# Performance work log

Hardware: AMD Instinct MI355X
Metric: run time of the kernel (lower is better)

Reference implementation:

```python
import jax, jax.numpy as jnp
import numpy as np

B = 65536   # batch (agent-timesteps)
NN = 16     # neighbors per agent
NO = 32     # obstacles per agent
SD = 4      # state_dim_per_agent
D_ROBOT = 0.3
D_OBST = 0.5
B_GAMMA = 0.01
B_EXPH = 1.0
A_MIN, A_MAX = -2.0, 2.0
PHI_MIN, PHI_MAX = -2.0, 2.0


def _mlp2(h, W1, b1, W2, b2):
    # DeepSet sub-network: activation between layers, linear last (matches
    # 'for layer in layers[:-1]: x = act(layer(x)); x = layers[-1](x)')
    return jax.nn.relu(h @ W1 + b1) @ W2 + b2


def setup_inputs() -> dict:
    key = jax.random.key(0)
    ks = jax.random.split(key, 24)
    own = jax.random.normal(ks[0], (B, SD), dtype=jnp.float32)
    # relative positions with |component| in [0.5, 2.0] so norms exceed D_* (barrier well-defined)
    npos = jax.random.uniform(ks[1], (B, NN, 2), minval=0.5, maxval=2.0) * jnp.sign(jax.random.normal(ks[2], (B, NN, 2)))
    nvel = 0.1 * jax.random.normal(ks[3], (B, NN, 2))
    neigh = jnp.concatenate([npos, nvel], axis=-1).reshape(B, 4 * NN)
    opos = (jax.random.uniform(ks[4], (B, NO, 2), minval=0.5, maxval=2.0) * jnp.sign(jax.random.normal(ks[5], (B, NO, 2)))).reshape(B, 2 * NO)
    x = jnp.concatenate([jnp.full((B, 1), float(NN), dtype=jnp.float32), own, neigh, opos], axis=1)
    noise = 0.05 * jax.random.normal(ks[6], (B, 2), dtype=jnp.float32)  # the 0.05*N(0,1) action noise, made deterministic

    def lin(k, i, o):
        return 0.1 * jax.random.normal(k, (i, o), dtype=jnp.float32)

    return {
        'x': x, 'noise': noise,
        # neighbor DeepSet: phi 4->64->16, rho 16->64->8
        'pnW1': lin(ks[7], 4, 64),  'pnb1': jnp.zeros((64,), jnp.float32),
        'pnW2': lin(ks[8], 64, 16), 'pnb2': jnp.zeros((16,), jnp.float32),
        'rnW1': lin(ks[9], 16, 64), 'rnb1': jnp.zeros((64,), jnp.float32),
        'rnW2': lin(ks[10], 64, 8), 'rnb2': jnp.zeros((8,), jnp.float32),
        # obstacle DeepSet: phi 2->64->16, rho 16->64->8
        'poW1': lin(ks[11], 2, 64),  'pob1': jnp.zeros((64,), jnp.float32),
        'poW2': lin(ks[12], 64, 16), 'pob2': jnp.zeros((16,), jnp.float32),
        'roW1': lin(ks[13], 16, 64), 'rob1': jnp.zeros((64,), jnp.float32),
        'roW2': lin(ks[14], 64, 8),  'rob2': jnp.zeros((8,), jnp.float32),
        # psi: 18 -> 64 -> 64 -> 2
        'psW1': lin(ks[15], 18, 64), 'psb1': jnp.zeros((64,), jnp.float32),
        'psW2': lin(ks[16], 64, 64), 'psb2': jnp.zeros((64,), jnp.float32),
        'psW3': lin(ks[17], 64, 2),  'psb3': jnp.zeros((2,), jnp.float32),
    }


def reference(x, noise,
              pnW1, pnb1, pnW2, pnb2, rnW1, rnb1, rnW2, rnb2,
              poW1, pob1, poW2, pob2, roW1, rob1, roW2, rob2,
              psW1, psb1, psW2, psb2, psW3, psb3):
    b = x.shape[0]
    neigh = x[:, 5:5 + 4 * NN].reshape(b, NN, 4)   # per-neighbor relative state
    obst = x[:, 5 + 4 * NN:].reshape(b, NO, 2)      # per-obstacle relative pos

    # 'empty' (learned) action: DeepSets + psi MLP
    rho_n = _mlp2(_mlp2(neigh, pnW1, pnb1, pnW2, pnb2).sum(axis=1), rnW1, rnb1, rnW2, rnb2)
    rho_o = _mlp2(_mlp2(obst, poW1, pob1, poW2, pob2).sum(axis=1), roW1, rob1, roW2, rob2)
    g = x[:, 1:3]
    h = jnp.concatenate([rho_n, rho_o, g], axis=1)
    h = jax.nn.relu(h @ psW1 + psb1)
    h = jax.nn.relu(h @ psW2 + psb2)
    h = jnp.tanh(h @ psW3 + psb3)
    empty = (h + 1.0) / 2.0 * (PHI_MAX - PHI_MIN) + PHI_MIN

    # barrier terms, vectorized over all neighbors/obstacles at once:
    # A = b_gamma * P * ||P||^-1 * (||P|| - D)^(-b_exph), summed over edges
    def barrier_sum(P, D):
        nrm = jnp.linalg.norm(P, axis=-1, keepdims=True)   # [b, E, 1]
        H = nrm - D
        return (B_GAMMA * P / (nrm * H ** B_EXPH)).sum(axis=1)

    bar = barrier_sum(-neigh[..., :2], D_ROBOT) + barrier_sum(-obst, D_OBST)

    a = jnp.tanh(empty + bar + noise)
    return (a + 1.0) / 2.0 * (A_MAX - A_MIN) + A_MIN
```

## Files before the change

### kernel.cpp

```cpp
#include <hip/hip_runtime.h>

#define NN 16
#define NO 32
#define XCOLS 133

typedef _Float16 h8v __attribute__((ext_vector_type(8)));
typedef _Float16 h2 __attribute__((ext_vector_type(2)));
typedef float f4v __attribute__((ext_vector_type(4)));
typedef unsigned ui4 __attribute__((ext_vector_type(4)));
typedef float f2u __attribute__((ext_vector_type(2), aligned(4)));

static __device__ __forceinline__ f4v MFMA(h8v a, h8v b, f4v c) {
    return __builtin_amdgcn_mfma_f32_16x16x32_f16(a, b, c, 0, 0, 0);
}
static __device__ __forceinline__ unsigned pkbits(float a, float b) {
    return __builtin_bit_cast(unsigned, __builtin_amdgcn_cvt_pkrtz(a, b));
}
static __device__ __forceinline__ h2 u2h(unsigned v) { return __builtin_bit_cast(h2, v); }

__global__ void prep_frags(
    const float* __restrict__ pnW1, const float* __restrict__ pnW2,
    const float* __restrict__ rnW1, const float* __restrict__ rnW2,
    const float* __restrict__ poW1, const float* __restrict__ poW2,
    const float* __restrict__ roW1, const float* __restrict__ roW2,
    const float* __restrict__ psW1, const float* __restrict__ psW2,
    const float* __restrict__ psW3, unsigned* __restrict__ ws)
{
    const float* Ws[11] = {pnW1,pnW2,rnW1,rnW2,poW1,poW2,roW1,roW2,psW1,psW2,psW3};
    const int Kr[11]   = {4,64,16,64,2,64,16,64,18,64,64};
    const int Nr[11]   = {64,16,64,8,64,16,64,8,64,64,2};
    const int nkc[11]  = {1,2,1,2,1,2,1,2,1,2,2};
    const int nnt[11]  = {4,1,4,1,4,1,4,1,4,4,1};
    const int base[11] = {0,1024,1536,2560,3072,4096,4608,5632,6144,7168,9216};

    const int gid = blockIdx.x * 256 + threadIdx.x;
    int start = 0;
    #pragma unroll
    for (int a2 = 0; a2 < 11; ++a2) {
        const int n = nkc[a2] * nnt[a2] * 256;
        if (gid >= start && gid < start + n) {
            const int i = gid - start;
            const float* Wm = Ws[a2];
            const int K = Kr[a2], N = Nr[a2], nt_n = nnt[a2];
            const int d = i & 3, lane = (i >> 2) & 63, t = i >> 8;
            const int nt = t % nt_n, kc = t / nt_n;
            const int k = kc * 32 + 8 * (lane >> 4) + 2 * d;
            const int col = nt * 16 + (lane & 15);
            const float v0 = (k     < K && col < N) ? Wm[(k    ) * N + col] : 0.f;
            const float v1 = (k + 1 < K && col < N) ? Wm[(k + 1) * N + col] : 0.f;
            ws[base[a2] + i] = pkbits(v0, v1);
        }
        start += n;
    }
}

__global__ __launch_bounds__(64, 4) void barrier_net_kernel(
    const float* __restrict__ x, const float* __restrict__ noise,
    const float* __restrict__ pnb1, const float* __restrict__ pnb2,
    const float* __restrict__ rnb1, const float* __restrict__ rnb2,
    const float* __restrict__ pob1, const float* __restrict__ pob2,
    const float* __restrict__ rob1, const float* __restrict__ rob2,
    const float* __restrict__ psb1, const float* __restrict__ psb2,
    const float* __restrict__ psb3,
    const unsigned* __restrict__ wsu, float* __restrict__ out)
{
    __shared__ unsigned XS[16 * 66];
    __shared__ _Float16 W[3136];

    const int l = threadIdx.x;
    const int r = l & 15;
    const int g = l >> 4;
    const int eb = blockIdx.x * 16;

    float* barf = (float*)(W + 3072);
    const h8v* FB = (const h8v*)wsu;

    {
        const float* base = x + (size_t)eb * XCOLS;
        f2u raw[16];
        #pragma unroll
        for (int it = 0; it < 16; ++it)
            raw[it] = *(const f2u*)(base + (size_t)it * XCOLS + 5 + 2 * l);
        f2u graw = {0.f, 0.f};
        if (l < 16) graw = *(const f2u*)(base + (size_t)l * XCOLS + 1);
        #pragma unroll
        for (int it = 0; it < 16; ++it)
            XS[it * 66 + l] = pkbits(raw[it][0], raw[it][1]);
        if (l < 16) XS[l * 66 + 64] = pkbits(graw[0], graw[1]);
    }

    {
        unsigned* z = (unsigned*)(W + 2048);
        #pragma unroll
        for (int i = 0; i < 8; ++i) z[l + 64 * i] = 0u;
    }

    const int rowb = r * 66;
    const int sw8 = (r & 7) << 3;
    const int sw4 = (r & 3) << 3;

    {
        float bq0 = 0.f, bq1 = 0.f;
        #pragma unroll
        for (int jj = 0; jj < 4; ++jj) {
            const h2 v = u2h(XS[rowb + 2 * (4 * g + jj)]);
            const float v0 = (float)v[0], v1 = (float)v[1];
            const float nrm = sqrtf(v0*v0 + v1*v1);
            const float cc = 0.01f * __builtin_amdgcn_rcpf(nrm * (nrm - 0.3f));
            bq0 -= cc * v0; bq1 -= cc * v1;
        }
        #pragma unroll
        for (int jj = 0; jj < 8; ++jj) {
            const h2 v = u2h(XS[rowb + 32 + 8 * g + jj]);
            const float v0 = (float)v[0], v1 = (float)v[1];
            const float nrm = sqrtf(v0*v0 + v1*v1);
            const float cc = 0.01f * __builtin_amdgcn_rcpf(nrm * (nrm - 0.5f));
            bq0 -= cc * v0; bq1 -= cc * v1;
        }
        bq0 += __shfl_xor(bq0, 16); bq0 += __shfl_xor(bq0, 32);
        bq1 += __shfl_xor(bq1, 16); bq1 += __shfl_xor(bq1, 32);
        if (g == 0) { barf[2*r] = bq0; barf[2*r + 1] = bq1; }
    }

    {
        const h8v B0 = FB[0*64 + l], B1 = FB[1*64 + l];
        const h8v B2 = FB[2*64 + l], B3 = FB[3*64 + l];
        const f4v c0 = {pnb1[r], pnb1[r], pnb1[r], pnb1[r]};
        const f4v c1 = {pnb1[16+r], pnb1[16+r], pnb1[16+r], pnb1[16+r]};
        const f4v c2 = {pnb1[32+r], pnb1[32+r], pnb1[32+r], pnb1[32+r]};
        const f4v c3 = {pnb1[48+r], pnb1[48+r], pnb1[48+r], pnb1[48+r]};
        f4v s0 = {0,0,0,0}, s1 = {0,0,0,0}, s2 = {0,0,0,0}, s3 = {0,0,0,0};
        #pragma unroll 4
        for (int j = 0; j < NN; ++j) {
            const uint2 np = *(const uint2*)&XS[rowb + 2 * j];
            ui4 au = {np.x, np.y, 0u, 0u};
            const h8v a = __builtin_bit_cast(h8v, au);
            const f4v d0 = MFMA(a, B0, c0);
            const f4v d1 = MFMA(a, B1, c1);
            const f4v d2 = MFMA(a, B2, c2);
            const f4v d3 = MFMA(a, B3, c3);
            #pragma unroll
            for (int q = 0; q < 4; ++q) {
                s0[q] += fmaxf(d0[q], 0.f); s1[q] += fmaxf(d1[q], 0.f);
                s2[q] += fmaxf(d2[q], 0.f); s3[q] += fmaxf(d3[q], 0.f);
            }
        }
        #pragma unroll
        for (int q = 0; q < 4; ++q) {
            const int e = 4 * g + q;
            const int m = (e & 7) << 3;
            W[e*64 + (( 0 + r) ^ m)] = (_Float16)s0[q];
            W[e*64 + ((16 + r) ^ m)] = (_Float16)s1[q];
            W[e*64 + ((32 + r) ^ m)] = (_Float16)s2[q];
            W[e*64 + ((48 + r) ^ m)] = (_Float16)s3[q];
        }
    }

    {
        const h8v B0 = FB[768 + 0*64 + l], B1 = FB[768 + 1*64 + l];
        const h8v B2 = FB[768 + 2*64 + l], B3 = FB[768 + 3*64 + l];
        const f4v c0 = {pob1[r], pob1[r], pob1[r], pob1[r]};
        const f4v c1 = {pob1[16+r], pob1[16+r], pob1[16+r], pob1[16+r]};
        const f4v c2 = {pob1[32+r], pob1[32+r], pob1[32+r], pob1[32+r]};
        const f4v c3 = {pob1[48+r], pob1[48+r], pob1[48+r], pob1[48+r]};
        f4v s0 = {0,0,0,0}, s1 = {0,0,0,0}, s2 = {0,0,0,0}, s3 = {0,0,0,0};
        #pragma unroll 2
        for (int t = 0; t < 16; ++t) {
            const uint2 op = *(const uint2*)&XS[rowb + 32 + 2 * t];
            ui4 au0 = {op.x, 0u, 0u, 0u};
            ui4 au1 = {op.y, 0u, 0u, 0u};
            const h8v a0 = __builtin_bit_cast(h8v, au0);
            const h8v a1 = __builtin_bit_cast(h8v, au1);
            const f4v d0 = MFMA(a0, B0, c0); const f4v e0 = MFMA(a1, B0, c0);
            const f4v d1 = MFMA(a0, B1, c1); const f4v e1 = MFMA(a1, B1, c1);
            const f4v d2 = MFMA(a0, B2, c2); const f4v e2 = MFMA(a1, B2, c2);
            const f4v d3 = MFMA(a0, B3, c3); const f4v e3 = MFMA(a1, B3, c3);
            #pragma unroll
            for (int q = 0; q < 4; ++q) {
                s0[q] += fmaxf(d0[q], 0.f) + fmaxf(e0[q], 0.f);
                s1[q] += fmaxf(d1[q], 0.f) + fmaxf(e1[q], 0.f);
                s2[q] += fmaxf(d2[q], 0.f) + fmaxf(e2[q], 0.f);
                s3[q] += fmaxf(d3[q], 0.f) + fmaxf(e3[q], 0.f);
            }
        }
        #pragma unroll
        for (int q = 0; q < 4; ++q) {
            const int e = 4 * g + q;
            const int m = (e & 7) << 3;
            W[1024 + e*64 + (( 0 + r) ^ m)] = (_Float16)s0[q];
            W[1024 + e*64 + ((16 + r) ^ m)] = (_Float16)s1[q];
            W[1024 + e*64 + ((32 + r) ^ m)] = (_Float16)s2[q];
            W[1024 + e*64 + ((48 + r) ^ m)] = (_Float16)s3[q];
        }
    }

    {
        h8v a0 = *(const h8v*)&W[r*64 + (( 0 + 8*g) ^ sw8)];
        h8v a1 = *(const h8v*)&W[r*64 + ((32 + 8*g) ^ sw8)];
        h8v b0 = FB[256 + 0*64 + l];
        h8v b1 = FB[256 + 1*64 + l];
        const float bb = 16.f * pnb2[r];
        f4v c = {bb, bb, bb, bb};
        f4v d = MFMA(a1, b1, MFMA(a0, b0, c));
        #pragma unroll
        for (int q = 0; q < 4; ++q) {
            const int row = 4 * g + q;
            W[2048 + row*32 + (r ^ ((row&3)<<3))] = (_Float16)d[q];
        }
    }
    {
        h8v a = *(const h8v*)&W[2048 + r*32 + ((8*g) ^ sw4)];
        #pragma unroll
        for (int nt = 0; nt < 4; ++nt) {
            h8v b = FB[384 + nt*64 + l];
            const float bb = rnb1[16*nt + r];
            f4v c = {bb, bb, bb, bb};
            f4v d = MFMA(a, b, c);
            #pragma unroll
            for (int q = 0; q < 4; ++q) {
                const int row = 4 * g + q;
                W[row*64 + ((16*nt + r) ^ ((row&7)<<3))] = (_Float16)fmaxf(d[q], 0.f);
            }
        }
    }
    {
        h8v a0 = *(const h8v*)&W[r*64 + (( 0 + 8*g) ^ sw8)];
        h8v a1 = *(const h8v*)&W[r*64 + ((32 + 8*g) ^ sw8)];
        h8v b0 = FB[640 + 0*64 + l];
        h8v b1 = FB[640 + 1*64 + l];
        const float bb = (r < 8) ? rnb2[r & 7] : 0.f;
        f4v c = {bb, bb, bb, bb};
        f4v d = MFMA(a1, b1, MFMA(a0, b0, c));
        if (r < 8) {
            #pragma unroll
            for (int q = 0; q < 4; ++q) {
                const int row = 4 * g + q;
                W[2560 + row*32 + (r ^ ((row&3)<<3))] = (_Float16)d[q];
            }
        }
    }
    {
        h8v a0 = *(const h8v*)&W[1024 + r*64 + (( 0 + 8*g) ^ sw8)];
        h8v a1 = *(const h8v*)&W[1024 + r*64 + ((32 + 8*g) ^ sw8)];
        h8v b0 = FB[1024 + 0*64 + l];
        h8v b1 = FB[1024 + 1*64 + l];
        const float bb = 32.f * pob2[r];
        f4v c = {bb, bb, bb, bb};
        f4v d = MFMA(a1, b1, MFMA(a0, b0, c));
        #pragma unroll
        for (int q = 0; q < 4; ++q) {
            const int row = 4 * g + q;
            W[2048 + row*32 + (r ^ ((row&3)<<3))] = (_Float16)d[q];
        }
    }
    {
        h8v a = *(const h8v*)&W[2048 + r*32 + ((8*g) ^ sw4)];
        #pragma unroll
        for (int nt = 0; nt < 4; ++nt) {
            h8v b = FB[1152 + nt*64 + l];
            const float bb = rob1[16*nt + r];
            f4v c = {bb, bb, bb, bb};
            f4v d = MFMA(a, b, c);
            #pragma unroll
            for (int q = 0; q < 4; ++q) {
                const int row = 4 * g + q;
                W[row*64 + ((16*nt + r) ^ ((row&7)<<3))] = (_Float16)fmaxf(d[q], 0.f);
            }
        }
    }
    {
        h8v a0 = *(const h8v*)&W[r*64 + (( 0 + 8*g) ^ sw8)];
        h8v a1 = *(const h8v*)&W[r*64 + ((32 + 8*g) ^ sw8)];
        h8v b0 = FB[1408 + 0*64 + l];
        h8v b1 = FB[1408 + 1*64 + l];
        const float bb = (r < 8) ? rob2[r & 7] : 0.f;
        f4v c = {bb, bb, bb, bb};
        f4v d = MFMA(a1, b1, MFMA(a0, b0, c));
        if (r < 8) {
            #pragma unroll
            for (int q = 0; q < 4; ++q) {
                const int row = 4 * g + q;
                W[2560 + row*32 + ((8 + r) ^ ((row&3)<<3))] = (_Float16)d[q];
            }
        }
    }
    if (g == 0) {
        const h2 gv = u2h(XS[rowb + 64]);
        W[2560 + r*32 + (16 ^ sw4)] = gv[0];
        W[2560 + r*32 + (17 ^ sw4)] = gv[1];
    }
    {
        h8v a = *(const h8v*)&W[2560 + r*32 + ((8*g) ^ sw4)];
        #pragma unroll
        for (int nt = 0; nt < 4; ++nt) {
            h8v b = FB[1536 + nt*64 + l];
            const float bb = psb1[16*nt + r];
            f4v c = {bb, bb, bb, bb};
            f4v d = MFMA(a, b, c);
            #pragma unroll
            for (int q = 0; q < 4; ++q) {
                const int row = 4 * g + q;
                W[1024 + row*64 + ((16*nt + r) ^ ((row&7)<<3))] = (_Float16)fmaxf(d[q], 0.f);
            }
        }
    }
    {
        h8v a0 = *(const h8v*)&W[1024 + r*64 + (( 0 + 8*g) ^ sw8)];
        h8v a1 = *(const h8v*)&W[1024 + r*64 + ((32 + 8*g) ^ sw8)];
        #pragma unroll
        for (int nt = 0; nt < 4; ++nt) {
            h8v b0 = FB[1792 + (0*4 + nt)*64 + l];
            h8v b1 = FB[1792 + (1*4 + nt)*64 + l];
            const float bb = psb2[16*nt + r];
            f4v c = {bb, bb, bb, bb};
            f4v d = MFMA(a1, b1, MFMA(a0, b0, c));
            #pragma unroll
            for (int q = 0; q < 4; ++q) {
                const int row = 4 * g + q;
                W[row*64 + ((16*nt + r) ^ ((row&7)<<3))] = (_Float16)fmaxf(d[q], 0.f);
            }
        }
    }
    f4v dOut;
    {
        h8v a0 = *(const h8v*)&W[r*64 + (( 0 + 8*g) ^ sw8)];
        h8v a1 = *(const h8v*)&W[r*64 + ((32 + 8*g) ^ sw8)];
        h8v b0 = FB[2304 + 0*64 + l];
        h8v b1 = FB[2304 + 1*64 + l];
        const float bb = (r < 2) ? psb3[r & 1] : 0.f;
        f4v c = {bb, bb, bb, bb};
        dOut = MFMA(a1, b1, MFMA(a0, b0, c));
    }
    if (r < 2) {
        #pragma unroll
        for (int q = 0; q < 4; ++q) {
            const int e = 4 * g + q;
            const float o = dOut[q];
            const float bar = barf[e*2 + r];
            const float nz = noise[2 * (size_t)(eb + e) + r];
            const float av = tanhf(2.f * tanhf(o) + bar + nz);
            out[2 * (size_t)(eb + e) + r] = 2.f * av;
        }
    }
}

extern "C" void kernel_launch(void* const* d_in, const int* in_sizes, int n_in,
                              void* d_out, int out_size, void* d_ws, size_t ws_size,
                              hipStream_t stream) {
    const float* x    = (const float*)d_in[0];
    const float* nz   = (const float*)d_in[1];
    const float* pnW1 = (const float*)d_in[2];
    const float* pnb1 = (const float*)d_in[3];
    const float* pnW2 = (const float*)d_in[4];
    const float* pnb2 = (const float*)d_in[5];
    const float* rnW1 = (const float*)d_in[6];
    const float* rnb1 = (const float*)d_in[7];
    const float* rnW2 = (const float*)d_in[8];
    const float* rnb2 = (const float*)d_in[9];
    const float* poW1 = (const float*)d_in[10];
    const float* pob1 = (const float*)d_in[11];
    const float* poW2 = (const float*)d_in[12];
    const float* pob2 = (const float*)d_in[13];
    const float* roW1 = (const float*)d_in[14];
    const float* rob1 = (const float*)d_in[15];
    const float* roW2 = (const float*)d_in[16];
    const float* rob2 = (const float*)d_in[17];
    const float* psW1 = (const float*)d_in[18];
    const float* psb1 = (const float*)d_in[19];
    const float* psW2 = (const float*)d_in[20];
    const float* psb2 = (const float*)d_in[21];
    const float* psW3 = (const float*)d_in[22];
    const float* psb3 = (const float*)d_in[23];

    unsigned* ws = (unsigned*)d_ws;
    hipLaunchKernelGGL(prep_frags, dim3(38), dim3(256), 0, stream,
        pnW1, pnW2, rnW1, rnW2, poW1, poW2, roW1, roW2, psW1, psW2, psW3, ws);

    const int b = in_sizes[0] / XCOLS;
    hipLaunchKernelGGL(barrier_net_kernel, dim3(b / 16), dim3(64), 0, stream,
        x, nz, pnb1, pnb2, rnb1, rnb2, pob1, pob2, rob1, rob2,
        psb1, psb2, psb3, ws, (float*)d_out);
}
```

Baseline: 44.68 us.

## Split each 16-agent tile across two wavefronts with barrier-synchronized stages

Each block now runs two wavefronts on the same 16 agents. The phi-layer MFMA column tiles, the barrier sums and the psi layers are split between them, and the neighbor and obstacle rho branches run in parallel, one on each wave. The aim is to shorten the serial per-wave MFMA chain and add latency hiding. The cost is several __syncthreads, a larger shared buffer, and idle half-waves during the final single-wave stage.

```diff
diff --git a/kernel.cpp b/kernel.cpp
--- a/kernel.cpp
+++ b/kernel.cpp
@@ -54,7 +54,16 @@
     }
 }
 
-__global__ __launch_bounds__(64, 4) void barrier_net_kernel(
+#define SN  0
+#define SO  1024
+#define PNN 2048
+#define PNO 2560
+#define HBF 3072
+#define BARA 3584
+#define BARB 3648
+#define XSF 3712
+
+__global__ __launch_bounds__(128, 8) void barrier_net_kernel(
     const float* __restrict__ x, const float* __restrict__ noise,
     const float* __restrict__ pnb1, const float* __restrict__ pnb2,
     const float* __restrict__ rnb1, const float* __restrict__ rnb2,
@@ -64,54 +73,72 @@
     const float* __restrict__ psb3,
     const unsigned* __restrict__ wsu, float* __restrict__ out)
 {
-    __shared__ unsigned XS[16 * 66];
-    __shared__ _Float16 W[3136];
-
-    const int l = threadIdx.x;
+    __shared__ _Float16 S[5824];
+    unsigned* XS = (unsigned*)S + (XSF / 2);
+    float* barfA = (float*)(S + BARA);
+    float* barfB = (float*)(S + BARB);
+
+    const int tid = threadIdx.x;
+    const int l = tid & 63;
+    const int w = tid >> 6;
     const int r = l & 15;
     const int g = l >> 4;
     const int eb = blockIdx.x * 16;
 
-    float* barf = (float*)(W + 3072);
     const h8v* FB = (const h8v*)wsu;
-
-    {
-        const float* base = x + (size_t)eb * XCOLS;
-        f2u raw[16];
-        #pragma unroll
-        for (int it = 0; it < 16; ++it)
-            raw[it] = *(const f2u*)(base + (size_t)it * XCOLS + 5 + 2 * l);
-        f2u graw = {0.f, 0.f};
-        if (l < 16) graw = *(const f2u*)(base + (size_t)l * XCOLS + 1);
-        #pragma unroll
-        for (int it = 0; it < 16; ++it)
-            XS[it * 66 + l] = pkbits(raw[it][0], raw[it][1]);
-        if (l < 16) XS[l * 66 + 64] = pkbits(graw[0], graw[1]);
-    }
-
-    {
-        unsigned* z = (unsigned*)(W + 2048);
-        #pragma unroll
-        for (int i = 0; i < 8; ++i) z[l + 64 * i] = 0u;
-    }
-
-    const int rowb = r * 66;
     const int sw8 = (r & 7) << 3;
     const int sw4 = (r & 3) << 3;
+    const int nt0 = 2 * w, nt1 = 2 * w + 1;
+
+    {
+        unsigned* z = (unsigned*)(S + PNN);
+        #pragma unroll
+        for (int i = 0; i < 6; ++i) z[tid + 128 * i] = 0u;
+    }
+    {
+        const float* base = x + (size_t)eb * XCOLS;
+        f2u raw[8];
+        #pragma unroll
+        for (int i = 0; i < 8; ++i) {
+            const int idx = i * 128 + tid;
+            const int ee = idx >> 6, cp = idx & 63;
+            raw[i] = *(const f2u*)(base + (size_t)ee * XCOLS + 5 + 2 * cp);
+        }
+        #pragma unroll
+        for (int i = 0; i < 8; ++i) {
+            const int idx = i * 128 + tid;
+            const int ee = idx >> 6, cp = idx & 63;
+            XS[ee * 66 + cp] = pkbits(raw[i][0], raw[i][1]);
+        }
+        if (tid < 16) {
+            const f2u graw = *(const f2u*)(base + (size_t)tid * XCOLS + 1);
+            XS[tid * 66 + 64] = pkbits(graw[0], graw[1]);
+        }
+    }
+    __syncthreads();
+
+    const int rowb = r * 66;
+
+    if (tid < 16) {
+        const h2 gv = u2h(XS[tid * 66 + 64]);
+        const int m = (tid & 3) << 3;
+        S[HBF + tid * 32 + (16 ^ m)] = gv[0];
+        S[HBF + tid * 32 + (17 ^ m)] = gv[1];
+    }
 
     {
         float bq0 = 0.f, bq1 = 0.f;
         #pragma unroll
-        for (int jj = 0; jj < 4; ++jj) {
-            const h2 v = u2h(XS[rowb + 2 * (4 * g + jj)]);
+        for (int jj = 0; jj < 2; ++jj) {
+            const h2 v = u2h(XS[rowb + 2 * (8 * w + 2 * g + jj)]);
             const float v0 = (float)v[0], v1 = (float)v[1];
             const float nrm = sqrtf(v0*v0 + v1*v1);
             const float cc = 0.01f * __builtin_amdgcn_rcpf(nrm * (nrm - 0.3f));
             bq0 -= cc * v0; bq1 -= cc * v1;
         }
         #pragma unroll
-        for (int jj = 0; jj < 8; ++jj) {
-            const h2 v = u2h(XS[rowb + 32 + 8 * g + jj]);
+        for (int jj = 0; jj < 4; ++jj) {
+            const h2 v = u2h(XS[rowb + 32 + 16 * w + 4 * g + jj]);
             const float v0 = (float)v[0], v1 = (float)v[1];
             const float nrm = sqrtf(v0*v0 + v1*v1);
             const float cc = 0.01f * __builtin_amdgcn_rcpf(nrm * (nrm - 0.5f));
@@ -119,17 +146,18 @@
         }
         bq0 += __shfl_xor(bq0, 16); bq0 += __shfl_xor(bq0, 32);
         bq1 += __shfl_xor(bq1, 16); bq1 += __shfl_xor(bq1, 32);
-        if (g == 0) { barf[2*r] = bq0; barf[2*r + 1] = bq1; }
-    }
-
-    {
-        const h8v B0 = FB[0*64 + l], B1 = FB[1*64 + l];
-        const h8v B2 = FB[2*64 + l], B3 = FB[3*64 + l];
-        const f4v c0 = {pnb1[r], pnb1[r], pnb1[r], pnb1[r]};
-        const f4v c1 = {pnb1[16+r], pnb1[16+r], pnb1[16+r], pnb1[16+r]};
-        const f4v c2 = {pnb1[32+r], pnb1[32+r], pnb1[32+r], pnb1[32+r]};
-        const f4v c3 = {pnb1[48+r], pnb1[48+r], pnb1[48+r], pnb1[48+r]};
-        f4v s0 = {0,0,0,0}, s1 = {0,0,0,0}, s2 = {0,0,0,0}, s3 = {0,0,0,0};
+        if (g == 0) {
+            float* bf = w ? barfB : barfA;
+            bf[2*r] = bq0; bf[2*r + 1] = bq1;
+        }
+    }
+
+    {
+        const h8v B0 = FB[nt0 * 64 + l], B1 = FB[nt1 * 64 + l];
+        const float b0s = pnb1[16*nt0 + r], b1s = pnb1[16*nt1 + r];
+        const f4v c0 = {b0s, b0s, b0s, b0s};
+        const f4v c1 = {b1s, b1s, b1s, b1s};
+        f4v s0 = {0,0,0,0}, s1 = {0,0,0,0};
         #pragma unroll 4
         for (int j = 0; j < NN; ++j) {
             const uint2 np = *(const uint2*)&XS[rowb + 2 * j];
@@ -137,178 +165,172 @@
             const h8v a = __builtin_bit_cast(h8v, au);
             const f4v d0 = MFMA(a, B0, c0);
             const f4v d1 = MFMA(a, B1, c1);
-            const f4v d2 = MFMA(a, B2, c2);
-            const f4v d3 = MFMA(a, B3, c3);
-            #pragma unroll
-            for (int q = 0; q < 4; ++q) {
-                s0[q] += fmaxf(d0[q], 0.f); s1[q] += fmaxf(d1[q], 0.f);
-                s2[q] += fmaxf(d2[q], 0.f); s3[q] += fmaxf(d3[q], 0.f);
+            #pragma unroll
+            for (int q = 0; q < 4; ++q) {
+                s0[q] += fmaxf(d0[q], 0.f);
+                s1[q] += fmaxf(d1[q], 0.f);
             }
         }
         #pragma unroll
         for (int q = 0; q < 4; ++q) {
             const int e = 4 * g + q;
             const int m = (e & 7) << 3;
-            W[e*64 + (( 0 + r) ^ m)] = (_Float16)s0[q];
-            W[e*64 + ((16 + r) ^ m)] = (_Float16)s1[q];
-            W[e*64 + ((32 + r) ^ m)] = (_Float16)s2[q];
-            W[e*64 + ((48 + r) ^ m)] = (_Float16)s3[q];
-        }
-    }
-
-    {
-        const h8v B0 = FB[768 + 0*64 + l], B1 = FB[768 + 1*64 + l];
-        const h8v B2 = FB[768 + 2*64 + l], B3 = FB[768 + 3*64 + l];
-        const f4v c0 = {pob1[r], pob1[r], pob1[r], pob1[r]};
-        const f4v c1 = {pob1[16+r], pob1[16+r], pob1[16+r], pob1[16+r]};
-        const f4v c2 = {pob1[32+r], pob1[32+r], pob1[32+r], pob1[32+r]};
-        const f4v c3 = {pob1[48+r], pob1[48+r], pob1[48+r], pob1[48+r]};
-        f4v s0 = {0,0,0,0}, s1 = {0,0,0,0}, s2 = {0,0,0,0}, s3 = {0,0,0,0};
+            S[SN + e*64 + ((16*nt0 + r) ^ m)] = (_Float16)s0[q];
+            S[SN + e*64 + ((16*nt1 + r) ^ m)] = (_Float16)s1[q];
+        }
+    }
+
+    {
+        const h8v B0 = FB[768 + nt0 * 64 + l], B1 = FB[768 + nt1 * 64 + l];
+        const float b0s = pob1[16*nt0 + r], b1s = pob1[16*nt1 + r];
+        const f4v c0 = {b0s, b0s, b0s, b0s};
+        const f4v c1 = {b1s, b1s, b1s, b1s};
+        f4v s0 = {0,0,0,0}, s1 = {0,0,0,0};
         #pragma unroll 2
         for (int t = 0; t < 16; ++t) {
             const uint2 op = *(const uint2*)&XS[rowb + 32 + 2 * t];
-            ui4 au0 = {op.x, 0u, 0u, 0u};
-            ui4 au1 = {op.y, 0u, 0u, 0u};
-            const h8v a0 = __builtin_bit_cast(h8v, au0);
-            const h8v a1 = __builtin_bit_cast(h8v, au1);
+            ui4 a0u = {op.x, 0u, 0u, 0u};
+            ui4 a1u = {op.y, 0u, 0u, 0u};
+            const h8v a0 = __builtin_bit_cast(h8v, a0u);
+            const h8v a1 = __builtin_bit_cast(h8v, a1u);
             const f4v d0 = MFMA(a0, B0, c0); const f4v e0 = MFMA(a1, B0, c0);
             const f4v d1 = MFMA(a0, B1, c1); const f4v e1 = MFMA(a1, B1, c1);
-            const f4v d2 = MFMA(a0, B2, c2); const f4v e2 = MFMA(a1, B2, c2);
-            const f4v d3 = MFMA(a0, B3, c3); const f4v e3 = MFMA(a1, B3, c3);
             #pragma unroll
             for (int q = 0; q < 4; ++q) {
                 s0[q] += fmaxf(d0[q], 0.f) + fmaxf(e0[q], 0.f);
                 s1[q] += fmaxf(d1[q], 0.f) + fmaxf(e1[q], 0.f);
-                s2[q] += fmaxf(d2[q], 0.f) + fmaxf(e2[q], 0.f);
-                s3[q] += fmaxf(d3[q], 0.f) + fmaxf(e3[q], 0.f);
             }
         }
         #pragma unroll
         for (int q = 0; q < 4; ++q) {
             const int e = 4 * g + q;
             const int m = (e & 7) << 3;
-            W[1024 + e*64 + (( 0 + r) ^ m)] = (_Float16)s0[q];
-            W[1024 + e*64 + ((16 + r) ^ m)] = (_Float16)s1[q];
-            W[1024 + e*64 + ((32 + r) ^ m)] = (_Float16)s2[q];
-            W[1024 + e*64 + ((48 + r) ^ m)] = (_Float16)s3[q];
-        }
-    }
-
-    {
-        h8v a0 = *(const h8v*)&W[r*64 + (( 0 + 8*g) ^ sw8)];
-        h8v a1 = *(const h8v*)&W[r*64 + ((32 + 8*g) ^ sw8)];
-        h8v b0 = FB[256 + 0*64 + l];
-        h8v b1 = FB[256 + 1*64 + l];
-        const float bb = 16.f * pnb2[r];
-        f4v c = {bb, bb, bb, bb};
-        f4v d = MFMA(a1, b1, MFMA(a0, b0, c));
+            S[SO + e*64 + ((16*nt0 + r) ^ m)] = (_Float16)s0[q];
+            S[SO + e*64 + ((16*nt1 + r) ^ m)] = (_Float16)s1[q];
+        }
+    }
+    __syncthreads();
+
+    if (w == 0) {
+        {
+            h8v a0 = *(const h8v*)&S[SN + r*64 + (( 0 + 8*g) ^ sw8)];
+            h8v a1 = *(const h8v*)&S[SN + r*64 + ((32 + 8*g) ^ sw8)];
+            h8v b0 = FB[256 + 0*64 + l];
+            h8v b1 = FB[256 + 1*64 + l];
+            const float bb = 16.f * pnb2[r];
+            f4v c = {bb, bb, bb, bb};
+            f4v d = MFMA(a1, b1, MFMA(a0, b0, c));
+            #pragma unroll
+            for (int q = 0; q < 4; ++q) {
+                const int row = 4 * g + q;
+                S[PNN + row*32 + (r ^ ((row&3)<<3))] = (_Float16)d[q];
+            }
+        }
+        {
+            h8v a = *(const h8v*)&S[PNN + r*32 + ((8*g) ^ sw4)];
+            #pragma unroll
+            for (int nt = 0; nt < 4; ++nt) {
+                h8v b = FB[384 + nt*64 + l];
+                const float bb = rnb1[16*nt + r];
+                f4v c = {bb, bb, bb, bb};
+                f4v d = MFMA(a, b, c);
+                #pragma unroll
+                for (int q = 0; q < 4; ++q) {
+                    const int row = 4 * g + q;
+                    S[SN + row*64 + ((16*nt + r) ^ ((row&7)<<3))] = (_Float16)fmaxf(d[q], 0.f);
+                }
+            }
+        }
+        {
+            h8v a0 = *(const h8v*)&S[SN + r*64 + (( 0 + 8*g) ^ sw8)];
+            h8v a1 = *(const h8v*)&S[SN + r*64 + ((32 + 8*g) ^ sw8)];
+            h8v b0 = FB[640 + 0*64 + l];
+            h8v b1 = FB[640 + 1*64 + l];
+            const float bb = (r < 8) ? rnb2[r & 7] : 0.f;
+            f4v c = {bb, bb, bb, bb};
+            f4v d = MFMA(a1, b1, MFMA(a0, b0, c));
+            if (r < 8) {
+                #pragma unroll
+                for (int q = 0; q < 4; ++q) {
+                    const int row = 4 * g + q;
+                    S[HBF + row*32 + (r ^ ((row&3)<<3))] = (_Float16)d[q];
+                }
+            }
+        }
+    } else {
+        {
+            h8v a0 = *(const h8v*)&S[SO + r*64 + (( 0 + 8*g) ^ sw8)];
+            h8v a1 = *(const h8v*)&S[SO + r*64 + ((32 + 8*g) ^ sw8)];
+            h8v b0 = FB[1024 + 0*64 + l];
+            h8v b1 = FB[1024 + 1*64 + l];
+            const float bb = 32.f * pob2[r];
+            f4v c = {bb, bb, bb, bb};
+            f4v d = MFMA(a1, b1, MFMA(a0, b0, c));
+            #pragma unroll
+            for (int q = 0; q < 4; ++q) {
+                const int row = 4 * g + q;
+                S[PNO + row*32 + (r ^ ((row&3)<<3))] = (_Float16)d[q];
+            }
+        }
+        {
+            h8v a = *(const h8v*)&S[PNO + r*32 + ((8*g) ^ sw4)];
+            #pragma unroll
+            for (int nt = 0; nt < 4; ++nt) {
+                h8v b = FB[1152 + nt*64 + l];
+                const float bb = rob1[16*nt + r];
+                f4v c = {bb, bb, bb, bb};
+                f4v d = MFMA(a, b, c);
+                #pragma unroll
+                for (int q = 0; q < 4; ++q) {
+                    const int row = 4 * g + q;
+                    S[SO + row*64 + ((16*nt + r) ^ ((row&7)<<3))] = (_Float16)fmaxf(d[q], 0.f);
+                }
+            }
+        }
+        {
+            h8v a0 = *(const h8v*)&S[SO + r*64 + (( 0 + 8*g) ^ sw8)];
+            h8v a1 = *(const h8v*)&S[SO + r*64 + ((32 + 8*g) ^ sw8)];
+            h8v b0 = FB[1408 + 0*64 + l];
+            h8v b1 = FB[1408 + 1*64 + l];
+            const float bb = (r < 8) ? rob2[r & 7] : 0.f;
+            f4v c = {bb, bb, bb, bb};
+            f4v d = MFMA(a1, b1, MFMA(a0, b0, c));
+            if (r < 8) {
+                #pragma unroll
+                for (int q = 0; q < 4; ++q) {
+                    const int row = 4 * g + q;
+                    S[HBF + row*32 + ((8 + r) ^ ((row&3)<<3))] = (_Float16)d[q];
+                }
+            }
+        }
+    }
+    __syncthreads();
+
+    {
+        h8v a = *(const h8v*)&S[HBF + r*32 + ((8*g) ^ sw4)];
+        h8v b0 = FB[1536 + nt0*64 + l];
+        h8v b1 = FB[1536 + nt1*64 + l];
+        const float b0s = psb1[16*nt0 + r], b1s = psb1[16*nt1 + r];
+        f4v c0 = {b0s, b0s, b0s, b0s};
+        f4v c1 = {b1s, b1s, b1s, b1s};
+        f4v d0 = MFMA(a, b0, c0);
+        f4v d1 = MFMA(a, b1, c1);
         #pragma unroll
         for (int q = 0; q < 4; ++q) {
             const int row = 4 * g + q;
-            W[2048 + row*32 + (r ^ ((row&3)<<3))] = (_Float16)d[q];
-        }
-    }
-    {
-        h8v a = *(const h8v*)&W[2048 + r*32 + ((8*g) ^ sw4)];
-        #pragma unroll
-        for (int nt = 0; nt < 4; ++nt) {
-            h8v b = FB[384 + nt*64 + l];
-            const float bb = rnb1[16*nt + r];
-            f4v c = {bb, bb, bb, bb};
-            f4v d = MFMA(a, b, c);
-            #pragma unroll
-            for (int q = 0; q < 4; ++q) {
-                const int row = 4 * g + q;
-                W[row*64 + ((16*nt + r) ^ ((row&7)<<3))] = (_Float16)fmaxf(d[q], 0.f);
-            }
-        }
-    }
-    {
-        h8v a0 = *(const h8v*)&W[r*64 + (( 0 + 8*g) ^ sw8)];
-        h8v a1 = *(const h8v*)&W[r*64 + ((32 + 8*g) ^ sw8)];
-        h8v b0 = FB[640 + 0*64 + l];
-        h8v b1 = FB[640 + 1*64 + l];
-        const float bb = (r < 8) ? rnb2[r & 7] : 0.f;
-        f4v c = {bb, bb, bb, bb};
-        f4v d = MFMA(a1, b1, MFMA(a0, b0, c));
-        if (r < 8) {
-            #pragma unroll
-            for (int q = 0; q < 4; ++q) {
-                const int row = 4 * g + q;
-                W[2560 + row*32 + (r ^ ((row&3)<<3))] = (_Float16)d[q];
-            }
-        }
-    }
-    {
-        h8v a0 = *(const h8v*)&W[1024 + r*64 + (( 0 + 8*g) ^ sw8)];
-        h8v a1 = *(const h8v*)&W[1024 + r*64 + ((32 + 8*g) ^ sw8)];
-        h8v b0 = FB[1024 + 0*64 + l];
-        h8v b1 = FB[1024 + 1*64 + l];
-        const float bb = 32.f * pob2[r];
-        f4v c = {bb, bb, bb, bb};
-        f4v d = MFMA(a1, b1, MFMA(a0, b0, c));
-        #pragma unroll
-        for (int q = 0; q < 4; ++q) {
-            const int row = 4 * g + q;
-            W[2048 + row*32 + (r ^ ((row&3)<<3))] = (_Float16)d[q];
-        }
-    }
-    {
-        h8v a = *(const h8v*)&W[2048 + r*32 + ((8*g) ^ sw4)];
-        #pragma unroll
-        for (int nt = 0; nt < 4; ++nt) {
-            h8v b = FB[1152 + nt*64 + l];
-            const float bb = rob1[16*nt + r];
-            f4v c = {bb, bb, bb, bb};
-            f4v d = MFMA(a, b, c);
-            #pragma unroll
-            for (int q = 0; q < 4; ++q) {
-                const int row = 4 * g + q;
-                W[row*64 + ((16*nt + r) ^ ((row&7)<<3))] = (_Float16)fmaxf(d[q], 0.f);
-            }
-        }
-    }
-    {
-        h8v a0 = *(const h8v*)&W[r*64 + (( 0 + 8*g) ^ sw8)];
-        h8v a1 = *(const h8v*)&W[r*64 + ((32 + 8*g) ^ sw8)];
-        h8v b0 = FB[1408 + 0*64 + l];
-        h8v b1 = FB[1408 + 1*64 + l];
-        const float bb = (r < 8) ? rob2[r & 7] : 0.f;
-        f4v c = {bb, bb, bb, bb};
-        f4v d = MFMA(a1, b1, MFMA(a0, b0, c));
-        if (r < 8) {
-            #pragma unroll
-            for (int q = 0; q < 4; ++q) {
-                const int row = 4 * g + q;
-                W[2560 + row*32 + ((8 + r) ^ ((row&3)<<3))] = (_Float16)d[q];
-            }
-        }
-    }
-    if (g == 0) {
-        const h2 gv = u2h(XS[rowb + 64]);
-        W[2560 + r*32 + (16 ^ sw4)] = gv[0];
-        W[2560 + r*32 + (17 ^ sw4)] = gv[1];
-    }
-    {
-        h8v a = *(const h8v*)&W[2560 + r*32 + ((8*g) ^ sw4)];
-        #pragma unroll
-        for (int nt = 0; nt < 4; ++nt) {
-            h8v b = FB[1536 + nt*64 + l];
-            const float bb = psb1[16*nt + r];
-            f4v c = {bb, bb, bb, bb};
-            f4v d = MFMA(a, b, c);
-            #pragma unroll
-            for (int q = 0; q < 4; ++q) {
-                const int row = 4 * g + q;
-                W[1024 + row*64 + ((16*nt + r) ^ ((row&7)<<3))] = (_Float16)fmaxf(d[q], 0.f);
-            }
-        }
-    }
-    {
-        h8v a0 = *(const h8v*)&W[1024 + r*64 + (( 0 + 8*g) ^ sw8)];
-        h8v a1 = *(const h8v*)&W[1024 + r*64 + ((32 + 8*g) ^ sw8)];
-        #pragma unroll
-        for (int nt = 0; nt < 4; ++nt) {
+            const int m = (row & 7) << 3;
+            S[SN + row*64 + ((16*nt0 + r) ^ m)] = (_Float16)fmaxf(d0[q], 0.f);
+            S[SN + row*64 + ((16*nt1 + r) ^ m)] = (_Float16)fmaxf(d1[q], 0.f);
+        }
+    }
+    __syncthreads();
+
+    {
+        h8v a0 = *(const h8v*)&S[SN + r*64 + (( 0 + 8*g) ^ sw8)];
+        h8v a1 = *(const h8v*)&S[SN + r*64 + ((32 + 8*g) ^ sw8)];
+        #pragma unroll
+        for (int i = 0; i < 2; ++i) {
+            const int nt = 2 * w + i;
             h8v b0 = FB[1792 + (0*4 + nt)*64 + l];
             h8v b1 = FB[1792 + (1*4 + nt)*64 + l];
             const float bb = psb2[16*nt + r];
@@ -317,29 +339,30 @@
             #pragma unroll
             for (int q = 0; q < 4; ++q) {
                 const int row = 4 * g + q;
-                W[row*64 + ((16*nt + r) ^ ((row&7)<<3))] = (_Float16)fmaxf(d[q], 0.f);
-            }
-        }
-    }
-    f4v dOut;
-    {
-        h8v a0 = *(const h8v*)&W[r*64 + (( 0 + 8*g) ^ sw8)];
-        h8v a1 = *(const h8v*)&W[r*64 + ((32 + 8*g) ^ sw8)];
+                S[SO + row*64 + ((16*nt + r) ^ ((row&7)<<3))] = (_Float16)fmaxf(d[q], 0.f);
+            }
+        }
+    }
+    __syncthreads();
+
+    if (w == 0) {
+        h8v a0 = *(const h8v*)&S[SO + r*64 + (( 0 + 8*g) ^ sw8)];
+        h8v a1 = *(const h8v*)&S[SO + r*64 + ((32 + 8*g) ^ sw8)];
         h8v b0 = FB[2304 + 0*64 + l];
         h8v b1 = FB[2304 + 1*64 + l];
         const float bb = (r < 2) ? psb3[r & 1] : 0.f;
         f4v c = {bb, bb, bb, bb};
-        dOut = MFMA(a1, b1, MFMA(a0, b0, c));
-    }
-    if (r < 2) {
-        #pragma unroll
-        for (int q = 0; q < 4; ++q) {
-            const int e = 4 * g + q;
-            const float o = dOut[q];
-            const float bar = barf[e*2 + r];
-            const float nz = noise[2 * (size_t)(eb + e) + r];
-            const float av = tanhf(2.f * tanhf(o) + bar + nz);
-            out[2 * (size_t)(eb + e) + r] = 2.f * av;
+        f4v dOut = MFMA(a1, b1, MFMA(a0, b0, c));
+        if (r < 2) {
+            #pragma unroll
+            for (int q = 0; q < 4; ++q) {
+                const int e = 4 * g + q;
+                const float o = dOut[q];
+                const float bar = barfA[e*2 + r] + barfB[e*2 + r];
+                const float nz = noise[2 * (size_t)(eb + e) + r];
+                const float av = tanhf(2.f * tanhf(o) + bar + nz);
+                out[2 * (size_t)(eb + e) + r] = 2.f * av;
+            }
         }
     }
 }
@@ -377,7 +400,7 @@
         pnW1, pnW2, rnW1, rnW2, poW1, poW2, roW1, roW2, psW1, psW2, psW3, ws);
 
     const int b = in_sizes[0] / XCOLS;
-    hipLaunchKernelGGL(barrier_net_kernel, dim3(b / 16), dim3(64), 0, stream,
+    hipLaunchKernelGGL(barrier_net_kernel, dim3(b / 16), dim3(128), 0, stream,
         x, nz, pnb1, pnb2, rnb1, rnb2, pob1, pob2, rob1, rob2,
         psb1, psb2, psb3, ws, (float*)d_out);
 }
```

Measured after the change: 48.96 us. +9.6%, slower.
